# Kernel optimization log

Measured on AMD Instinct MI355X. Metric: run time of the kernel, lower is better.

## Reference

```python
import jax, jax.numpy as jnp
import numpy as np

DN = ('NCHW', 'OIHW', 'NCHW')
BN_EPS = 1e-5
R = 2  # local Gaussian refinement radius


def conv(x, w):
    pad = 'SAME' if w.shape[2] > 1 else 'VALID'
    return jax.lax.conv_general_dilated(x, w, (1, 1), pad, dimension_numbers=DN)


def bn_relu(x, g, b):
    # inference BatchNorm with running_mean=0, running_var=1 (fresh module stats)
    scale = (g / jnp.sqrt(1.0 + BN_EPS))[None, :, None, None]
    return jax.nn.relu(x * scale + b[None, :, None, None])


def soft_argmax(hm):
    # beta = 1.0
    B, K, H, W = hm.shape
    p = jax.nn.softmax(hm.reshape(B, K, H * W), axis=-1).reshape(B, K, H, W)
    xc = jnp.einsum('bkhw,w->bk', p, jnp.arange(W, dtype=hm.dtype))
    yc = jnp.einsum('bkhw,h->bk', p, jnp.arange(H, dtype=hm.dtype))
    scores = hm.reshape(B, K, -1).max(-1)
    return jnp.stack([xc, yc], -1), scores


def local_refine(hm, coords):
    # vectorized version of the per-(b,k) python loop: masked 5x5 window softmax
    B, K, H, W = hm.shape
    n = 2 * R + 1
    px = jnp.round(jnp.clip(coords[..., 0], 0, W - 1)).astype(jnp.int32)  # (B,K)
    py = jnp.round(jnp.clip(coords[..., 1], 0, H - 1)).astype(jnp.int32)
    d = jnp.arange(-R, R + 1)
    xs = px[..., None] + d  # (B,K,n)
    ys = py[..., None] + d
    mask = ((ys >= 0) & (ys < H))[..., :, None] & ((xs >= 0) & (xs < W))[..., None, :]
    xc = jnp.clip(xs, 0, W - 1); yc = jnp.clip(ys, 0, H - 1)
    bb = jnp.arange(B)[:, None, None, None]; kk = jnp.arange(K)[None, :, None, None]
    patch = hm[bb, kk, yc[:, :, :, None], xc[:, :, None, :]]  # (B,K,n,n)
    w = jax.nn.softmax(jnp.where(mask, patch, -jnp.inf).reshape(B, K, n * n), -1).reshape(B, K, n, n)
    rx = (w * xc[:, :, None, :].astype(hm.dtype)).sum((-2, -1))
    ry = (w * yc[:, :, :, None].astype(hm.dtype)).sum((-2, -1))
    return jnp.stack([rx, ry], -1)


def sample_offsets(off, coords):
    # F.grid_sample bilinear, padding_mode='border', align_corners=True,
    # one sample point per (b,k); normalization round-trips to pixel coords.
    B, K, _, H, W = off.shape
    ix = jnp.clip(coords[..., 0], 0, W - 1); iy = jnp.clip(coords[..., 1], 0, H - 1)
    x0 = jnp.floor(ix); y0 = jnp.floor(iy)
    wx = (ix - x0)[..., None]; wy = (iy - y0)[..., None]
    x0i = jnp.clip(x0.astype(jnp.int32), 0, W - 1); x1i = jnp.clip(x0i + 1, 0, W - 1)
    y0i = jnp.clip(y0.astype(jnp.int32), 0, H - 1); y1i = jnp.clip(y0i + 1, 0, H - 1)
    bb = jnp.arange(B)[:, None]; kk = jnp.arange(K)[None, :]
    v00 = off[bb, kk, :, y0i, x0i]; v01 = off[bb, kk, :, y0i, x1i]
    v10 = off[bb, kk, :, y1i, x0i]; v11 = off[bb, kk, :, y1i, x1i]
    return (1 - wy) * ((1 - wx) * v00 + wx * v01) + wy * ((1 - wx) * v10 + wx * v11)


def setup_inputs() -> dict:
    key = jax.random.key(0)
    B, C, H, W = 32, 256, 64, 64
    HID, K = 256, 17
    ks = iter(jax.random.split(key, 16))
    def kw(shape):
        fan_out = shape[0] * shape[2] * shape[3]
        return jax.random.normal(next(ks), shape, jnp.float32) * np.sqrt(2.0 / fan_out).astype(np.float32)
    return {
        'x': jax.random.normal(next(ks), (B, C, H, W), jnp.float32),
        'w_s1': kw((HID, C, 3, 3)), 'g_s1': jnp.ones(HID), 'b_s1': jnp.zeros(HID),
        'w_s2': kw((HID, HID, 3, 3)), 'g_s2': jnp.ones(HID), 'b_s2': jnp.zeros(HID),
        'w_h1': kw((HID, HID, 3, 3)), 'g_h1': jnp.ones(HID), 'b_h1': jnp.zeros(HID),
        'w_h2': kw((K, HID, 1, 1)), 'c_h2': jnp.zeros(K),
        'w_o1': kw((HID, HID, 3, 3)), 'g_o1': jnp.ones(HID), 'b_o1': jnp.zeros(HID),
        'w_o2': kw((2 * K, HID, 1, 1)), 'c_o2': jnp.zeros(2 * K),
        'w_v1': kw((HID // 2, HID, 3, 3)), 'g_v1': jnp.ones(HID // 2), 'b_v1': jnp.zeros(HID // 2),
        'w_v2': kw((K, HID // 2, 1, 1)), 'c_v2': jnp.zeros(K),
        'alpha': jnp.float32(0.5), 'fusion': jnp.float32(0.5),
    }


def reference(x, w_s1, g_s1, b_s1, w_s2, g_s2, b_s2, w_h1, g_h1, b_h1, w_h2, c_h2,
              w_o1, g_o1, b_o1, w_o2, c_o2, w_v1, g_v1, b_v1, w_v2, c_v2, alpha, fusion):
    B = x.shape[0]; K = w_h2.shape[0]
    s = bn_relu(conv(x, w_s1), g_s1, b_s1)
    s = bn_relu(conv(s, w_s2), g_s2, b_s2)
    heat = conv(bn_relu(conv(s, w_h1), g_h1, b_h1), w_h2) + c_h2[None, :, None, None]
    off = conv(bn_relu(conv(s, w_o1), g_o1, b_o1), w_o2) + c_o2[None, :, None, None]
    H, W = off.shape[2], off.shape[3]
    off = off.reshape(B, K, 2, H, W)
    var = jax.nn.softplus(conv(bn_relu(conv(s, w_v1), g_v1, b_v1), w_v2) + c_v2[None, :, None, None])
    fw = jax.nn.sigmoid(fusion)
    # decode path (SubPixelRefinement + offset correction)
    cg, scores = soft_argmax(heat)
    cl = local_refine(heat, cg)
    a = jax.nn.sigmoid(alpha)
    coords = a * cg + (1 - a) * cl
    coords = coords + fw * sample_offsets(off, coords)
    return heat, off, var, fw, coords, scores
```

## Files before the change

### kernel.cpp

```cpp
#include <hip/hip_runtime.h>
#include <hip/hip_bf16.h>
#include <math.h>

#define B_  32
#define C_  256
#define H_  64
#define W_  64
#define K_  17
#define HW_ 4096

#define HEAT_OFF  0
#define OFF_OFF   2228224
#define VAR_OFF   6684672
#define FW_OFF    8912896
#define COORD_OFF 8912897
#define SCORE_OFF 8913985

#define BN_SCALE 0.9999950000374997f

typedef __attribute__((ext_vector_type(8))) short  bf16x8;
typedef __attribute__((ext_vector_type(4))) float  f32x4;

__device__ __forceinline__ unsigned short f2bf(float x) {
  unsigned int u = __float_as_uint(x);
  u = u + 0x7fffu + ((u >> 16) & 1u);
  return (unsigned short)(u >> 16);
}
__device__ __forceinline__ float bf2f(unsigned short h) {
  return __uint_as_float(((unsigned int)h) << 16);
}

__device__ __forceinline__ void gload16(const void* g, void* l) {
  __builtin_amdgcn_global_load_lds(
      (const __attribute__((address_space(1))) void*)g,
      (__attribute__((address_space(3))) void*)l, 16, 0, 0);
}

#define SZP_ELEMS  35684352ull
#define SZP_BYTES  71368704ull
#define XP_HI   0ull
#define XP_LO   71368704ull
#define S1_HI   142737408ull
#define S1_LO   214106112ull
#define S2_HI   285474816ull
#define S2_LO   356843520ull
#define WP_BASE 428212224ull
#define WS1_HI  (WP_BASE)
#define WS1_LO  (WP_BASE + 1179648ull)
#define WS2_HI  (WP_BASE + 2359296ull)
#define WS2_LO  (WP_BASE + 3538944ull)
#define WH1_HI  (WP_BASE + 4718592ull)
#define WH1_LO  (WP_BASE + 5898240ull)
#define WO1_HI  (WP_BASE + 7077888ull)
#define WO1_LO  (WP_BASE + 8257536ull)
#define WV1_HI  (WP_BASE + 9437184ull)
#define WV1_LO  (WP_BASE + 10027008ull)
#define CG_OFF  (WP_BASE + 10616832ull)

__global__ __launch_bounds__(256) void pack_x(
    const float* __restrict__ x, unsigned short* __restrict__ hi,
    unsigned short* __restrict__ lo) {
  __shared__ float s[128 * 66];
  const int b  = blockIdx.x / 66;
  const int pr = blockIdx.x % 66;
  const size_t obase = ((size_t)(b * 66 + pr) * 66) * 256;
  if (pr == 0 || pr == 65) {
    for (int i = threadIdx.x; i < 66 * 256; i += 256) { hi[obase + i] = 0; lo[obase + i] = 0; }
    return;
  }
  const int y = pr - 1;
  for (int h = 0; h < 2; ++h) {
    __syncthreads();
    for (int i = threadIdx.x; i < 128 * 66; i += 256) {
      int c = i / 66, pc = i % 66;
      int xx = pc - 1;
      float v = (xx >= 0 && xx < 64)
          ? x[((size_t)b * 256 + h * 128 + c) * 4096 + y * 64 + xx] : 0.f;
      s[i] = v;
    }
    __syncthreads();
    for (int i = threadIdx.x; i < 66 * 128; i += 256) {
      int pc = i / 128, c = i % 128;
      float v = s[c * 66 + pc];
      unsigned short hb = f2bf(v);
      size_t o = obase + (size_t)pc * 256 + h * 128 + c;
      hi[o] = hb;
      lo[o] = f2bf(v - bf2f(hb));
    }
  }
}

__global__ void pack_w(const float* __restrict__ w, unsigned short* __restrict__ hi,
                       unsigned short* __restrict__ lo, int COUT) {
  int i = blockIdx.x * 256 + threadIdx.x;
  int tot = COUT * 256 * 9;
  if (i >= tot) return;
  int co = i / (256 * 9);
  int r  = i - co * 256 * 9;
  int ci = r / 9;
  int k  = r - ci * 9;
  float v = w[i];
  unsigned short h = f2bf(v);
  size_t o = ((size_t)k * COUT + co) * 256 + ci;
  hi[o] = h;
  lo[o] = f2bf(v - bf2f(h));
}

__global__ void zero_border(unsigned short* __restrict__ hi, unsigned short* __restrict__ lo) {
  int i = blockIdx.x * 256 + threadIdx.x;
  if (i >= 32 * 260 * 256) return;
  int c = i & 255;
  int p = i >> 8;
  int b = p / 260;
  int q = p - b * 260;
  int pr, pc;
  if (q < 66) { pr = 0; pc = q; }
  else if (q < 132) { pr = 65; pc = q - 66; }
  else { int u = q - 132; pr = 1 + (u >> 1); pc = (u & 1) * 65; }
  size_t o = ((size_t)(b * 66 + pr) * 66 + pc) * 256 + c;
  hi[o] = 0; lo[o] = 0;
}

#define ABUF_BYTES 33792
#define BBASE      33792
#define BBUF_BYTES 16384
#define SMEM_SZ    66560

template <int COUT, int OUTMODE>
__global__ __launch_bounds__(256, 2) void conv3x3_mfma(
    const unsigned short* __restrict__ Phi, const unsigned short* __restrict__ Plo,
    const unsigned short* __restrict__ Whi, const unsigned short* __restrict__ Wlo,
    const float* __restrict__ gam, const float* __restrict__ bet,
    unsigned short* __restrict__ Ohi, unsigned short* __restrict__ Olo,
    float* __restrict__ Ofp) {
  const int mb   = blockIdx.x % 1024;
  const int nblk = blockIdx.x / 1024;

  const int b     = mb >> 5;
  const int ypair = mb & 31;
  const int Y     = ypair * 2;

  const int tid  = threadIdx.x;
  const int lane = tid & 63;
  const int wv   = tid >> 6;
  const int l15  = lane & 15;
  const int quad = lane >> 4;
  const int mhalf = (wv & 1) * 64;
  const int nbase = (wv >> 1) * 64;

  __shared__ __align__(16) char smem[SMEM_SZ];

  int pb[4];
#pragma unroll
  for (int mi = 0; mi < 4; ++mi) {
    int px = mhalf + mi * 16 + l15;
    pb[mi] = (px >> 6) * 66 + (px & 63);
  }
  int boffs[4];
#pragma unroll
  for (int ni = 0; ni < 4; ++ni) {
    int col = nbase + ni * 16 + l15;
    boffs[ni] = (col << 7) + (((quad ^ col) & 7) << 4);
  }

  f32x4 acc[4][4];
#pragma unroll
  for (int mi = 0; mi < 4; ++mi)
#pragma unroll
    for (int ni = 0; ni < 4; ++ni) acc[mi][ni] = (f32x4)0.f;

  const size_t ibase = ((size_t)(b * 66 + Y) * 66) * 256;

  auto dmaB = [&](int tt, int cc, int bsel) {
#pragma unroll
    for (int k = 0; k < 4; ++k) {
      int idx = k * 256 + tid;
      int co = idx >> 3, s7 = idx & 7;
      int hq = s7 ^ (co & 7);
      const unsigned short* src = (hq & 4) ? Wlo : Whi;
      const unsigned short* g = src + (size_t)tt * (COUT * 256)
                                + ((size_t)(nblk * 128 + co)) * 256 + cc * 32 + (hq & 3) * 8;
      char* l = smem + BBASE + bsel * BBUF_BYTES + (k * 256 + wv * 64) * 16;
      gload16(g, l);
    }
  };
  auto dmaA = [&](int cc) {
#pragma unroll
    for (int j = 0; j < 9; ++j) {
      if (j * 4 + wv < 33) {
        int idx = j * 256 + tid;
        int p = idx >> 3, s7 = idx & 7;
        int hq = s7 ^ (p & 7);
        const unsigned short* src = (hq & 4) ? Plo : Phi;
        const unsigned short* g = src + ibase + (size_t)p * 256 + (hq & 3) * 8 + cc * 32;
        char* l = smem + (j * 256 + wv * 64) * 16;
        gload16(g, l);
      }
    }
  };

  dmaA(0);
  dmaB(0, 0, 0);
  __syncthreads();

  for (int c2 = 0; c2 < 8; c2 += 2) {
#pragma unroll
    for (int h = 0; h < 2; ++h) {
      const int c = c2 + h;
#pragma unroll
      for (int t = 0; t < 9; ++t) {
        const int par = (h + t) & 1;
        if (!(c == 7 && t == 8)) {
          int nt = (t == 8) ? 0 : t + 1;
          int nc = (t == 8) ? c + 1 : c;
          dmaB(nt, nc, par ^ 1);
        }
        const int dtap = (t / 3) * 66 + (t % 3);
        bf16x8 ah[4], al[4], bh[4], bl[4];
#pragma unroll
        for (int mi = 0; mi < 4; ++mi) {
          int p = pb[mi] + dtap;
          int a = (p << 7) + (((quad ^ p) & 7) << 4);
          ah[mi] = *(const bf16x8*)(smem + a);
          al[mi] = *(const bf16x8*)(smem + (a ^ 64));
        }
        const int bb = BBASE + par * BBUF_BYTES;
#pragma unroll
        for (int ni = 0; ni < 4; ++ni) {
          bh[ni] = *(const bf16x8*)(smem + bb + boffs[ni]);
          bl[ni] = *(const bf16x8*)(smem + bb + (boffs[ni] ^ 64));
        }
#pragma unroll
        for (int mi = 0; mi < 4; ++mi)
#pragma unroll
          for (int ni = 0; ni < 4; ++ni) {
            acc[mi][ni] = __builtin_amdgcn_mfma_f32_16x16x32_bf16(ah[mi], bh[ni], acc[mi][ni], 0, 0, 0);
            acc[mi][ni] = __builtin_amdgcn_mfma_f32_16x16x32_bf16(al[mi], bh[ni], acc[mi][ni], 0, 0, 0);
            acc[mi][ni] = __builtin_amdgcn_mfma_f32_16x16x32_bf16(ah[mi], bl[ni], acc[mi][ni], 0, 0, 0);
          }
        if (!(c == 7 && t == 8)) {
          __syncthreads();
          if (t == 8) {
            dmaA(c + 1);
            __syncthreads();
          }
        }
      }
    }
  }

  __syncthreads();
  float scn[4], bin[4];
#pragma unroll
  for (int ni = 0; ni < 4; ++ni) {
    int co = nblk * 128 + nbase + ni * 16 + l15;
    scn[ni] = gam[co] * BN_SCALE;
    bin[ni] = bet[co];
  }

  float* SL = (float*)smem;
#pragma unroll
  for (int pass = 0; pass < 2; ++pass) {
    if ((wv & 1) == pass) {
#pragma unroll
      for (int mi = 0; mi < 4; ++mi)
#pragma unroll
        for (int ni = 0; ni < 4; ++ni)
#pragma unroll
          for (int r = 0; r < 4; ++r) {
            int lpx = mi * 16 + quad * 4 + r;
            int co  = nbase + ni * 16 + l15;
            SL[lpx * 129 + co] = fmaxf(acc[mi][ni][r] * scn[ni] + bin[ni], 0.f);
          }
    }
    __syncthreads();
    if (OUTMODE == 0) {
#pragma unroll
      for (int it = 0; it < 4; ++it) {
        int u = it * 256 + tid;
        int lpx = u >> 4, oct = u & 15;
        const float* row = SL + lpx * 129 + oct * 8;
        __align__(16) unsigned short hs[8], ls[8];
#pragma unroll
        for (int j = 0; j < 8; ++j) {
          float v = row[j];
          unsigned short hb = f2bf(v);
          hs[j] = hb;
          ls[j] = f2bf(v - bf2f(hb));
        }
        size_t o = ((size_t)(b * 66 + Y + pass + 1) * 66 + lpx + 1) * 256 + nblk * 128 + oct * 8;
        *(uint4*)(Ohi + o) = *(const uint4*)hs;
        *(uint4*)(Olo + o) = *(const uint4*)ls;
      }
    } else {
#pragma unroll
      for (int it = 0; it < 4; ++it) {
        int u = it * 256 + tid;
        int coL = u >> 3, xo = u & 7;
        __align__(16) float vv[8];
#pragma unroll
        for (int j = 0; j < 8; ++j) vv[j] = SL[(xo * 8 + j) * 129 + coL];
        size_t o = ((size_t)(b * COUT + nblk * 128 + coL)) * 4096 + (size_t)(Y + pass) * 64 + xo * 8;
        *(uint4*)(Ofp + o)     = *(const uint4*)&vv[0];
        *(uint4*)(Ofp + o + 4) = *(const uint4*)&vv[4];
      }
    }
    __syncthreads();
  }
}

template <int CO, int CIN>
__global__ __launch_bounds__(256) void conv1x1_kernel(
    const float* __restrict__ in, const float* __restrict__ w,
    const float* __restrict__ bias, float* __restrict__ out, int do_softplus) {
  __shared__ float s_w[CO * CIN];
  const int b   = blockIdx.x >> 4;
  const int pix = ((blockIdx.x & 15) << 8) + threadIdx.x;
  for (int i = threadIdx.x; i < CO * CIN; i += 256) s_w[i] = w[i];
  __syncthreads();

  float acc[CO];
#pragma unroll
  for (int co = 0; co < CO; ++co) acc[co] = 0.f;

  const float* ip = in + (size_t)b * CIN * HW_ + pix;
  for (int ci = 0; ci < CIN; ++ci) {
    float v = ip[(size_t)ci * HW_];
#pragma unroll
    for (int co = 0; co < CO; ++co) acc[co] = fmaf(v, s_w[co * CIN + ci], acc[co]);
  }
  float* op = out + (size_t)b * CO * HW_ + pix;
#pragma unroll
  for (int co = 0; co < CO; ++co) {
    float x = acc[co] + bias[co];
    if (do_softplus) x = fmaxf(x, 0.f) + log1pf(expf(-fabsf(x)));
    op[(size_t)co * HW_] = x;
  }
}

__global__ __launch_bounds__(256) void soft_argmax_kernel(
    const float* __restrict__ heat, float* __restrict__ cg,
    float* __restrict__ scores) {
  const int bk = blockIdx.x;
  const float* h = heat + (size_t)bk * HW_;
  const int tid = threadIdx.x;
  __shared__ float sred[256];

  float v[16];
  float lmax = -INFINITY;
#pragma unroll
  for (int i = 0; i < 16; ++i) {
    v[i] = h[tid + (i << 8)];
    lmax = fmaxf(lmax, v[i]);
  }
  sred[tid] = lmax; __syncthreads();
  for (int s = 128; s > 0; s >>= 1) {
    if (tid < s) sred[tid] = fmaxf(sred[tid], sred[tid + s]);
    __syncthreads();
  }
  const float m = sred[0];
  __syncthreads();

  float s = 0.f, sx = 0.f, sy = 0.f;
#pragma unroll
  for (int i = 0; i < 16; ++i) {
    int idx = tid + (i << 8);
    float e = expf(v[i] - m);
    s += e;
    sx += e * (float)(idx & 63);
    sy += e * (float)(idx >> 6);
  }
  sred[tid] = s; __syncthreads();
  for (int st = 128; st > 0; st >>= 1) { if (tid < st) sred[tid] += sred[tid + st]; __syncthreads(); }
  const float S = sred[0]; __syncthreads();
  sred[tid] = sx; __syncthreads();
  for (int st = 128; st > 0; st >>= 1) { if (tid < st) sred[tid] += sred[tid + st]; __syncthreads(); }
  const float SX = sred[0]; __syncthreads();
  sred[tid] = sy; __syncthreads();
  for (int st = 128; st > 0; st >>= 1) { if (tid < st) sred[tid] += sred[tid + st]; __syncthreads(); }
  const float SY = sred[0];

  if (tid == 0) {
    cg[bk * 2]     = SX / S;
    cg[bk * 2 + 1] = SY / S;
    scores[bk]     = m;
  }
}

__global__ void refine_kernel(
    const float* __restrict__ heat, const float* __restrict__ off,
    const float* __restrict__ cg, const float* __restrict__ alpha_p,
    const float* __restrict__ fusion_p, float* __restrict__ coords_out,
    float* __restrict__ fw_out) {
  const int kp = blockIdx.x * 64 + threadIdx.x;
  const float fw = 1.f / (1.f + expf(-fusion_p[0]));
  if (kp == 0) fw_out[0] = fw;
  if (kp >= B_ * K_) return;

  const float a = 1.f / (1.f + expf(-alpha_p[0]));
  const float* h = heat + (size_t)kp * HW_;
  const float cgx = cg[kp * 2];
  const float cgy = cg[kp * 2 + 1];
  const int px = (int)rintf(fminf(fmaxf(cgx, 0.f), 63.f));
  const int py = (int)rintf(fminf(fmaxf(cgy, 0.f), 63.f));

  float vals[25];
  float m = -INFINITY;
#pragma unroll
  for (int dy = 0; dy < 5; ++dy) {
    int ya = py + dy - 2;
    int yc = min(max(ya, 0), 63);
#pragma unroll
    for (int dx = 0; dx < 5; ++dx) {
      int xa = px + dx - 2;
      int xc = min(max(xa, 0), 63);
      bool inb = (ya >= 0) && (ya < H_) && (xa >= 0) && (xa < W_);
      float val = inb ? h[yc * W_ + xc] : -INFINITY;
      vals[dy * 5 + dx] = val;
      m = fmaxf(m, val);
    }
  }
  float s = 0.f, rx = 0.f, ry = 0.f;
#pragma unroll
  for (int dy = 0; dy < 5; ++dy) {
    int ya = py + dy - 2;
    int yc = min(max(ya, 0), 63);
#pragma unroll
    for (int dx = 0; dx < 5; ++dx) {
      int xa = px + dx - 2;
      int xc = min(max(xa, 0), 63);
      float e = expf(vals[dy * 5 + dx] - m);
      s += e;
      rx += e * (float)xc;
      ry += e * (float)yc;
    }
  }
  rx /= s; ry /= s;

  float cx = a * cgx + (1.f - a) * rx;
  float cy = a * cgy + (1.f - a) * ry;

  const float ix = fminf(fmaxf(cx, 0.f), 63.f);
  const float iy = fminf(fmaxf(cy, 0.f), 63.f);
  const float x0 = floorf(ix), y0 = floorf(iy);
  const float wx = ix - x0, wy = iy - y0;
  const int x0i = min(max((int)x0, 0), 63);
  const int x1i = min(x0i + 1, 63);
  const int y0i = min(max((int)y0, 0), 63);
  const int y1i = min(y0i + 1, 63);

  float smp[2];
#pragma unroll
  for (int ch = 0; ch < 2; ++ch) {
    const float* oc = off + ((size_t)kp * 2 + ch) * HW_;
    float v00 = oc[y0i * W_ + x0i];
    float v01 = oc[y0i * W_ + x1i];
    float v10 = oc[y1i * W_ + x0i];
    float v11 = oc[y1i * W_ + x1i];
    smp[ch] = (1.f - wy) * ((1.f - wx) * v00 + wx * v01)
            + wy * ((1.f - wx) * v10 + wx * v11);
  }
  cx += fw * smp[0];
  cy += fw * smp[1];
  coords_out[kp * 2]     = cx;
  coords_out[kp * 2 + 1] = cy;
}

extern "C" void kernel_launch(void* const* d_in, const int* in_sizes, int n_in,
                              void* d_out, int out_size, void* d_ws, size_t ws_size,
                              hipStream_t stream) {
  const float* x    = (const float*)d_in[0];
  const float* w_s1 = (const float*)d_in[1];
  const float* g_s1 = (const float*)d_in[2];
  const float* b_s1 = (const float*)d_in[3];
  const float* w_s2 = (const float*)d_in[4];
  const float* g_s2 = (const float*)d_in[5];
  const float* b_s2 = (const float*)d_in[6];
  const float* w_h1 = (const float*)d_in[7];
  const float* g_h1 = (const float*)d_in[8];
  const float* b_h1 = (const float*)d_in[9];
  const float* w_h2 = (const float*)d_in[10];
  const float* c_h2 = (const float*)d_in[11];
  const float* w_o1 = (const float*)d_in[12];
  const float* g_o1 = (const float*)d_in[13];
  const float* b_o1 = (const float*)d_in[14];
  const float* w_o2 = (const float*)d_in[15];
  const float* c_o2 = (const float*)d_in[16];
  const float* w_v1 = (const float*)d_in[17];
  const float* g_v1 = (const float*)d_in[18];
  const float* b_v1 = (const float*)d_in[19];
  const float* w_v2 = (const float*)d_in[20];
  const float* c_v2 = (const float*)d_in[21];
  const float* alpha  = (const float*)d_in[22];
  const float* fusion = (const float*)d_in[23];

  float* out = (float*)d_out;
  char*  ws  = (char*)d_ws;

  unsigned short* xp_hi = (unsigned short*)(ws + XP_HI);
  unsigned short* xp_lo = (unsigned short*)(ws + XP_LO);
  unsigned short* s1_hi = (unsigned short*)(ws + S1_HI);
  unsigned short* s1_lo = (unsigned short*)(ws + S1_LO);
  unsigned short* s2_hi = (unsigned short*)(ws + S2_HI);
  unsigned short* s2_lo = (unsigned short*)(ws + S2_LO);
  unsigned short* ws1_hi = (unsigned short*)(ws + WS1_HI);
  unsigned short* ws1_lo = (unsigned short*)(ws + WS1_LO);
  unsigned short* ws2_hi = (unsigned short*)(ws + WS2_HI);
  unsigned short* ws2_lo = (unsigned short*)(ws + WS2_LO);
  unsigned short* wh1_hi = (unsigned short*)(ws + WH1_HI);
  unsigned short* wh1_lo = (unsigned short*)(ws + WH1_LO);
  unsigned short* wo1_hi = (unsigned short*)(ws + WO1_HI);
  unsigned short* wo1_lo = (unsigned short*)(ws + WO1_LO);
  unsigned short* wv1_hi = (unsigned short*)(ws + WV1_HI);
  unsigned short* wv1_lo = (unsigned short*)(ws + WV1_LO);
  float* F0  = (float*)(ws + 0);
  float* cgb = (float*)(ws + CG_OFF);

  dim3 blk(256);

  pack_x<<<32 * 66, blk, 0, stream>>>(x, xp_hi, xp_lo);
  pack_w<<<256 * 9, blk, 0, stream>>>(w_s1, ws1_hi, ws1_lo, 256);
  pack_w<<<256 * 9, blk, 0, stream>>>(w_s2, ws2_hi, ws2_lo, 256);
  pack_w<<<256 * 9, blk, 0, stream>>>(w_h1, wh1_hi, wh1_lo, 256);
  pack_w<<<256 * 9, blk, 0, stream>>>(w_o1, wo1_hi, wo1_lo, 256);
  pack_w<<<128 * 9, blk, 0, stream>>>(w_v1, wv1_hi, wv1_lo, 128);
  zero_border<<<8320, blk, 0, stream>>>(s1_hi, s1_lo);
  zero_border<<<8320, blk, 0, stream>>>(s2_hi, s2_lo);

  conv3x3_mfma<256, 0><<<2048, blk, 0, stream>>>(xp_hi, xp_lo, ws1_hi, ws1_lo,
                                                 g_s1, b_s1, s1_hi, s1_lo, nullptr);
  conv3x3_mfma<256, 0><<<2048, blk, 0, stream>>>(s1_hi, s1_lo, ws2_hi, ws2_lo,
                                                 g_s2, b_s2, s2_hi, s2_lo, nullptr);
  conv3x3_mfma<256, 1><<<2048, blk, 0, stream>>>(s2_hi, s2_lo, wh1_hi, wh1_lo,
                                                 g_h1, b_h1, nullptr, nullptr, F0);
  conv1x1_kernel<17, 256><<<512, blk, 0, stream>>>(F0, w_h2, c_h2, out + HEAT_OFF, 0);
  conv3x3_mfma<256, 1><<<2048, blk, 0, stream>>>(s2_hi, s2_lo, wo1_hi, wo1_lo,
                                                 g_o1, b_o1, nullptr, nullptr, F0);
  conv1x1_kernel<34, 256><<<512, blk, 0, stream>>>(F0, w_o2, c_o2, out + OFF_OFF, 0);
  conv3x3_mfma<128, 1><<<1024, blk, 0, stream>>>(s2_hi, s2_lo, wv1_hi, wv1_lo,
                                                 g_v1, b_v1, nullptr, nullptr, F0);
  conv1x1_kernel<17, 128><<<512, blk, 0, stream>>>(F0, w_v2, c_v2, out + VAR_OFF, 1);

  soft_argmax_kernel<<<544, blk, 0, stream>>>(out + HEAT_OFF, cgb, out + SCORE_OFF);
  refine_kernel<<<9, dim3(64), 0, stream>>>(out + HEAT_OFF, out + OFF_OFF, cgb,
                                            alpha, fusion,
                                            out + COORD_OFF, out + FW_OFF);
}
```

Baseline: 2.098 ms.

## Load conv weights directly from global into registers, dropping LDS B double-buffer

The 3x3 conv MFMA kernel no longer stages weight tiles through a double-buffered LDS region. Each wave now reads its bf16 hi/lo weight fragments straight from global memory (through the cache) every tap. This halves LDS use, so launch bounds are raised to allow 3 blocks per CU, and the per-tap barriers are removed, leaving synchronisation only around the activation reload per channel chunk. The cost is global-load latency sitting directly in front of the MFMAs with no prefetch, plus redundant weight reads across the waves that share columns.

After: 3.903 ms. +86.0%, slower.

```diff
diff --git a/kernel.cpp b/kernel.cpp
--- a/kernel.cpp
+++ b/kernel.cpp
@@ -121,13 +121,10 @@
   hi[o] = 0; lo[o] = 0;
 }
 
-#define ABUF_BYTES 33792
-#define BBASE      33792
-#define BBUF_BYTES 16384
-#define SMEM_SZ    66560
+#define SMEM_SZ 33792
 
 template <int COUT, int OUTMODE>
-__global__ __launch_bounds__(256, 2) void conv3x3_mfma(
+__global__ __launch_bounds__(256, 3) void conv3x3_mfma(
     const unsigned short* __restrict__ Phi, const unsigned short* __restrict__ Plo,
     const unsigned short* __restrict__ Whi, const unsigned short* __restrict__ Wlo,
     const float* __restrict__ gam, const float* __restrict__ bet,
@@ -156,12 +153,10 @@
     int px = mhalf + mi * 16 + l15;
     pb[mi] = (px >> 6) * 66 + (px & 63);
   }
-  int boffs[4];
-#pragma unroll
-  for (int ni = 0; ni < 4; ++ni) {
-    int col = nbase + ni * 16 + l15;
-    boffs[ni] = (col << 7) + (((quad ^ col) & 7) << 4);
-  }
+  int bo[4];
+#pragma unroll
+  for (int ni = 0; ni < 4; ++ni)
+    bo[ni] = (nblk * 128 + nbase + ni * 16 + l15) * 256 + quad * 8;
 
   f32x4 acc[4][4];
 #pragma unroll
@@ -171,19 +166,6 @@
 
   const size_t ibase = ((size_t)(b * 66 + Y) * 66) * 256;
 
-  auto dmaB = [&](int tt, int cc, int bsel) {
-#pragma unroll
-    for (int k = 0; k < 4; ++k) {
-      int idx = k * 256 + tid;
-      int co = idx >> 3, s7 = idx & 7;
-      int hq = s7 ^ (co & 7);
-      const unsigned short* src = (hq & 4) ? Wlo : Whi;
-      const unsigned short* g = src + (size_t)tt * (COUT * 256)
-                                + ((size_t)(nblk * 128 + co)) * 256 + cc * 32 + (hq & 3) * 8;
-      char* l = smem + BBASE + bsel * BBUF_BYTES + (k * 256 + wv * 64) * 16;
-      gload16(g, l);
-    }
-  };
   auto dmaA = [&](int cc) {
 #pragma unroll
     for (int j = 0; j < 9; ++j) {
@@ -200,52 +182,38 @@
   };
 
   dmaA(0);
-  dmaB(0, 0, 0);
   __syncthreads();
 
-  for (int c2 = 0; c2 < 8; c2 += 2) {
-#pragma unroll
-    for (int h = 0; h < 2; ++h) {
-      const int c = c2 + h;
-#pragma unroll
-      for (int t = 0; t < 9; ++t) {
-        const int par = (h + t) & 1;
-        if (!(c == 7 && t == 8)) {
-          int nt = (t == 8) ? 0 : t + 1;
-          int nc = (t == 8) ? c + 1 : c;
-          dmaB(nt, nc, par ^ 1);
+  for (int c = 0; c < 8; ++c) {
+#pragma unroll
+    for (int t = 0; t < 9; ++t) {
+      const size_t woff = (size_t)t * (COUT * 256) + (size_t)c * 32;
+      bf16x8 bh[4], bl[4], ah[4], al[4];
+#pragma unroll
+      for (int ni = 0; ni < 4; ++ni) bh[ni] = *(const bf16x8*)(Whi + woff + bo[ni]);
+#pragma unroll
+      for (int ni = 0; ni < 4; ++ni) bl[ni] = *(const bf16x8*)(Wlo + woff + bo[ni]);
+      const int dtap = (t / 3) * 66 + (t % 3);
+#pragma unroll
+      for (int mi = 0; mi < 4; ++mi) {
+        int p = pb[mi] + dtap;
+        int a = (p << 7) + (((quad ^ p) & 7) << 4);
+        ah[mi] = *(const bf16x8*)(smem + a);
+        al[mi] = *(const bf16x8*)(smem + (a ^ 64));
+      }
+#pragma unroll
+      for (int mi = 0; mi < 4; ++mi)
+#pragma unroll
+        for (int ni = 0; ni < 4; ++ni) {
+          acc[mi][ni] = __builtin_amdgcn_mfma_f32_16x16x32_bf16(ah[mi], bh[ni], acc[mi][ni], 0, 0, 0);
+          acc[mi][ni] = __builtin_amdgcn_mfma_f32_16x16x32_bf16(al[mi], bh[ni], acc[mi][ni], 0, 0, 0);
+          acc[mi][ni] = __builtin_amdgcn_mfma_f32_16x16x32_bf16(ah[mi], bl[ni], acc[mi][ni], 0, 0, 0);
         }
-        const int dtap = (t / 3) * 66 + (t % 3);
-        bf16x8 ah[4], al[4], bh[4], bl[4];
-#pragma unroll
-        for (int mi = 0; mi < 4; ++mi) {
-          int p = pb[mi] + dtap;
-          int a = (p << 7) + (((quad ^ p) & 7) << 4);
-          ah[mi] = *(const bf16x8*)(smem + a);
-          al[mi] = *(const bf16x8*)(smem + (a ^ 64));
-        }
-        const int bb = BBASE + par * BBUF_BYTES;
-#pragma unroll
-        for (int ni = 0; ni < 4; ++ni) {
-          bh[ni] = *(const bf16x8*)(smem + bb + boffs[ni]);
-          bl[ni] = *(const bf16x8*)(smem + bb + (boffs[ni] ^ 64));
-        }
-#pragma unroll
-        for (int mi = 0; mi < 4; ++mi)
-#pragma unroll
-          for (int ni = 0; ni < 4; ++ni) {
-            acc[mi][ni] = __builtin_amdgcn_mfma_f32_16x16x32_bf16(ah[mi], bh[ni], acc[mi][ni], 0, 0, 0);
-            acc[mi][ni] = __builtin_amdgcn_mfma_f32_16x16x32_bf16(al[mi], bh[ni], acc[mi][ni], 0, 0, 0);
-            acc[mi][ni] = __builtin_amdgcn_mfma_f32_16x16x32_bf16(ah[mi], bl[ni], acc[mi][ni], 0, 0, 0);
-          }
-        if (!(c == 7 && t == 8)) {
-          __syncthreads();
-          if (t == 8) {
-            dmaA(c + 1);
-            __syncthreads();
-          }
-        }
-      }
+    }
+    if (c < 7) {
+      __syncthreads();
+      dmaA(c + 1);
+      __syncthreads();
     }
   }
 
```
